# Optimization experiments

Hardware: AMD Instinct MI355X
Metric: run time of the kernel (lower is better)

Reference implementation:

```python
import jax, jax.numpy as jnp
import numpy as np

B, N, D, K, H, HID, ITERS = 16, 4096, 64, 8, 4, 256, 3
DH = D // H
EPS = 1e-5


def _ln(x, g, b):
    m = x.mean(-1, keepdims=True)
    v = x.var(-1, keepdims=True)
    return (x - m) / jnp.sqrt(v + EPS) * g + b


def setup_inputs() -> dict:
    ks = jax.random.split(jax.random.key(0), 16)
    s = 1.0 / np.sqrt(D)
    return {
        "embeddings": jax.random.normal(ks[0], (B, N, D), dtype=jnp.float32),
        "slots_mu": jax.random.normal(ks[1], (1, K, D), dtype=jnp.float32) * 0.1,
        "slots_logsigma": jax.random.normal(ks[2], (1, K, D), dtype=jnp.float32) * 0.1,
        "mixing_init": jnp.full((1, K), 1.0 / K, dtype=jnp.float32),
        "to_keys": jax.random.uniform(ks[3], (K, D, D), dtype=jnp.float32),
        "to_queries": jax.random.uniform(ks[4], (K, D, D), dtype=jnp.float32),
        "to_values": jax.random.uniform(ks[5], (K, D, D), dtype=jnp.float32),
        "w_ih": jax.random.uniform(ks[6], (3 * D, D), minval=-s, maxval=s),
        "w_hh": jax.random.uniform(ks[7], (3 * D, D), minval=-s, maxval=s),
        "b_ih": jax.random.uniform(ks[8], (3 * D,), minval=-s, maxval=s),
        "b_hh": jax.random.uniform(ks[9], (3 * D,), minval=-s, maxval=s),
        "w1": jax.random.uniform(ks[10], (HID, D), minval=-s, maxval=s),
        "b1": jnp.zeros((HID,), jnp.float32),
        "w2": jax.random.uniform(ks[11], (D, HID), minval=-1.0 / np.sqrt(HID), maxval=1.0 / np.sqrt(HID)),
        "b2": jnp.zeros((D,), jnp.float32),
        "ln_in_g": jnp.ones((D,), jnp.float32), "ln_in_b": jnp.zeros((D,), jnp.float32),
        "ln_sl_g": jnp.ones((D,), jnp.float32), "ln_sl_b": jnp.zeros((D,), jnp.float32),
        "ln_ff_g": jnp.ones((D,), jnp.float32), "ln_ff_b": jnp.zeros((D,), jnp.float32),
        "noise_init": jax.random.normal(ks[12], (B, K, D), dtype=jnp.float32),
        "noise_final": jax.random.normal(ks[13], (B, K, D), dtype=jnp.float32),
    }


def reference(embeddings, slots_mu, slots_logsigma, mixing_init, to_keys, to_queries,
              to_values, w_ih, w_hh, b_ih, b_hh, w1, b1, w2, b2,
              ln_in_g, ln_in_b, ln_sl_g, ln_sl_b, ln_ff_g, ln_ff_b,
              noise_init, noise_final):
    mu = jnp.broadcast_to(slots_mu, (B, K, D))
    sigma = jnp.broadcast_to(jnp.exp(slots_logsigma), (B, K, D))
    slots = mu + sigma * noise_init                              # [B,K,D]
    mixing = jnp.broadcast_to(mixing_init, (B, K))[:, :, None]   # [B,K,1]

    x = _ln(embeddings, ln_in_g, ln_in_b)                        # [B,N,D]
    keys = jnp.einsum('bne,ked->bknd', x, to_keys).reshape(B, K, N, H, DH)
    values = jnp.einsum('bne,ked->bknd', x, to_values).reshape(B, K, N, H, DH)
    sigma = sigma.reshape(B, K, H, DH)
    # torch.einsum('bkd,kdd->bkd') uses the DIAGONAL of to_queries
    qdiag = jnp.einsum('kdd->kd', to_queries)                    # [K,D]
    log_pi = -0.5 * D * np.log(2.0 * np.pi)

    attn_vis = None
    for _ in range(ITERS):
        slots_prev = slots
        s_ln = _ln(slots, ln_sl_g, ln_sl_b)
        queries = (s_ln * qdiag[None]).reshape(B, K, H, DH)      # [B,K,H,Dh]
        exponent = -0.5 * (keys - queries[:, :, None]) ** 2 / (sigma[:, :, None] ** 2 + EPS)
        log_scale = -jnp.log(jnp.clip(sigma, EPS, None))[:, :, None]  # [B,K,1,H,Dh]
        gll = jnp.log(mixing + EPS)[..., None] + (log_pi + log_scale + exponent).sum(-1)  # [B,K,N,H]
        attn = jax.nn.softmax(gll, axis=1) + EPS
        attn_vis = attn
        Nk = attn.sum(axis=(2, 3))[:, :, None]                   # [B,K,1]
        upd = jnp.einsum('bknh,bknhd->bkhd', attn, values).reshape(B, K, D)
        upd = (1.0 / Nk + EPS) * upd
        nq = upd.reshape(B, K, H, DH)                            # source overwrites new_queries with slot_updates
        sig2 = jnp.einsum('bknh,bknhd->bkhd', attn, (keys - nq[:, :, None]) ** 2).reshape(B, K, D)
        sigma = (jnp.sqrt(sig2 / Nk) + EPS).reshape(B, K, H, DH)
        mixing = Nk / N
        # GRUCell (torch gate order: reset, update, new)
        xg = upd.reshape(-1, D) @ w_ih.T + b_ih
        hg = slots_prev.reshape(-1, D) @ w_hh.T + b_hh
        xr, xz, xn = jnp.split(xg, 3, axis=-1)
        hr, hz, hn = jnp.split(hg, 3, axis=-1)
        r = jax.nn.sigmoid(xr + hr)
        z = jax.nn.sigmoid(xz + hz)
        n = jnp.tanh(xn + r * hn)
        slots = ((1.0 - z) * n + z * slots_prev.reshape(-1, D)).reshape(B, K, D)
        pre = _ln(slots, ln_ff_g, ln_ff_b)
        slots = slots + jax.nn.relu(pre @ w1.T + b1) @ w2.T + b2

    sigma = sigma.reshape(B, K, D)
    slots = slots + sigma * noise_final
    return slots, attn_vis
```

## Files before the change

### kernel.cpp

```cpp
#include <hip/hip_runtime.h>
#include <math.h>

#define B_ 16
#define N_ 4096
#define D_ 64
#define K_ 8
#define H_ 4
#define HID_ 256
#define ITERS_ 3
#define EPS_ 1e-5f

#define HTERM_ (-940.9930580015849f)

__device__ __forceinline__ float waveReduceSum64(float v) {
  v += __shfl_xor(v, 1);  v += __shfl_xor(v, 2);  v += __shfl_xor(v, 4);
  v += __shfl_xor(v, 8);  v += __shfl_xor(v, 16); v += __shfl_xor(v, 32);
  return v;
}
__device__ __forceinline__ float groupReduceSum16(float v) {
  v += __shfl_xor(v, 1); v += __shfl_xor(v, 2); v += __shfl_xor(v, 4);
  v += __shfl_xor(v, 8);
  return v;
}

template <int CTRL>
__device__ __forceinline__ float dpp_mov(float v) {
  return __int_as_float(__builtin_amdgcn_update_dpp(
      0, __float_as_int(v), CTRL, 0xF, 0xF, true));
}
__device__ __forceinline__ float row16Sum(float v) {
  v += dpp_mov<0xB1>(v);
  v += dpp_mov<0x4E>(v);
  v += dpp_mov<0x124>(v);
  v += dpp_mov<0x128>(v);
  return v;
}

__global__ __launch_bounds__(256) void key_kernel(const float* __restrict__ emb,
    const float* __restrict__ g_in, const float* __restrict__ b_in,
    const float* __restrict__ Wk, float* __restrict__ x,
    float* __restrict__ keys, int b0) {
  __shared__ float xst[64 * 68];
  __shared__ float wks[64 * 64];
  int n0 = blockIdx.x * 64;
  int bl = blockIdx.y;
  int tid = threadIdx.x;
  int wave = tid >> 6, lane = tid & 63;

  {
    const float* eb = emb + ((size_t)(b0 + bl) * N_ + n0 + wave * 16) * 64 + lane;
    float* xrow = x + ((size_t)bl * N_ + n0 + wave * 16) * 64 + lane;
    float gl = g_in[lane], bb = b_in[lane];
    #pragma unroll 4
    for (int r = 0; r < 16; ++r) {
      float e = eb[(size_t)r * 64];
      float s  = waveReduceSum64(e);
      float sq = waveReduceSum64(e * e);
      float mean = s * (1.0f / 64.0f);
      float var  = sq * (1.0f / 64.0f) - mean * mean;
      float xv = (e - mean) * rsqrtf(var + EPS_) * gl + bb;
      xst[lane * 68 + wave * 16 + r] = xv;
      xrow[(size_t)r * 64] = xv;
    }
  }

  int tr = tid >> 4, tc = tid & 15;
  int r0 = tr * 4, c0 = tc * 4;
  size_t outb = ((size_t)bl * N_ + n0) * 512;

  for (int k = 0; k < K_; ++k) {
    __syncthreads();
    const float4* wk4 = (const float4*)(Wk + (size_t)k * 4096);
    float4* wks4 = (float4*)wks;
    for (int i = tid; i < 1024; i += 256) wks4[i] = wk4[i];
    __syncthreads();

    float ak[4][4] = {{0.f}};
    #pragma unroll 8
    for (int kk = 0; kk < 64; ++kk) {
      float4 xq = *(const float4*)&xst[kk * 68 + r0];
      float4 wq = *(const float4*)&wks[kk * 64 + c0];
      float xv[4] = {xq.x, xq.y, xq.z, xq.w};
      float wc[4] = {wq.x, wq.y, wq.z, wq.w};
      #pragma unroll
      for (int i = 0; i < 4; ++i)
        #pragma unroll
        for (int j = 0; j < 4; ++j)
          ak[i][j] = fmaf(xv[i], wc[j], ak[i][j]);
    }
    size_t ob = outb + (size_t)k * 64;
    #pragma unroll
    for (int i = 0; i < 4; ++i) {
      float4 kq = make_float4(ak[i][0], ak[i][1], ak[i][2], ak[i][3]);
      *(float4*)&keys[ob + (size_t)(r0 + i) * 512 + c0] = kq;
    }
  }
}

__global__ void init_kernel(const float* __restrict__ mu, const float* __restrict__ lsig,
                            const float* __restrict__ mix0, const float* __restrict__ noise,
                            const float* __restrict__ tq,
                            const float* __restrict__ g_sl, const float* __restrict__ b_sl,
                            float* __restrict__ slots, float* __restrict__ q,
                            float* __restrict__ i2s, float* __restrict__ base,
                            float* __restrict__ S1, float* __restrict__ S2,
                            float* __restrict__ S0, float* __restrict__ T, int b0) {
  int bk = b0 * K_ + blockIdx.x;
  int lane = threadIdx.x;
  int k = bk & (K_ - 1);
  int kd = k * 64 + lane;
  float sg = expf(lsig[kd]);
  float s = mu[kd] + sg * noise[bk * 64 + lane];
  slots[bk * 64 + lane] = s;
  float su = waveReduceSum64(s);
  float sq = waveReduceSum64(s * s);
  float mean = su * (1.0f / 64.0f);
  float var  = sq * (1.0f / 64.0f) - mean * mean;
  float sl = (s - mean) * rsqrtf(var + EPS_) * g_sl[lane] + b_sl[lane];
  q[bk * 64 + lane] = sl * tq[k * 4096 + lane * 65];
  i2s[bk * 64 + lane] = 0.5f / (sg * sg + EPS_);
  float ls = -logf(fmaxf(sg, EPS_));
  float lss = groupReduceSum16(ls);
  if ((lane & 15) == 0)
    base[bk * 4 + (lane >> 4)] = logf(mix0[k] + EPS_) + HTERM_ + lss;
  S1[bk * 64 + lane] = 0.0f;
  S2[bk * 64 + lane] = 0.0f;
  T[bk * 256 + lane]       = 0.0f;
  T[bk * 256 + 64 + lane]  = 0.0f;
  T[bk * 256 + 128 + lane] = 0.0f;
  T[bk * 256 + 192 + lane] = 0.0f;
  if (lane < 4) S0[bk * 4 + lane] = 0.0f;
}

template <bool WRITE_ATTN>
__global__ __launch_bounds__(256, 4) void attn_kernel(
    const float* __restrict__ keys, const float* __restrict__ x,
    const float* __restrict__ q, const float* __restrict__ i2s, const float* __restrict__ base,
    float* __restrict__ S1, float* __restrict__ S2, float* __restrict__ S0,
    float* __restrict__ T, float* __restrict__ attn_out, int b0) {
  int bl = blockIdx.y;
  int bg = b0 + bl;
  int wave = threadIdx.x >> 6, lane = threadIdx.x & 63;
  int h = lane >> 4;
  int n0 = (blockIdx.x * 4 + wave) * 16;

  __shared__ float att_lds[4][K_][64];
  __shared__ float blk[3104];
  __shared__ float bv_lds[32];
  for (int i = threadIdx.x; i < 3104; i += 256) blk[i] = 0.0f;
  if (threadIdx.x < 32) bv_lds[threadIdx.x] = base[bg * 32 + threadIdx.x];

  float qv[K_], iv[K_];
  {
    const float* qp = q + bg * 512 + lane;
    const float* ip = i2s + bg * 512 + lane;
    #pragma unroll
    for (int k = 0; k < K_; ++k) { qv[k] = qp[k * 64]; iv[k] = ip[k * 64]; }
  }
  float s1a[K_] = {0.f}, s2a[K_] = {0.f};
  __syncthreads();

  const float* kptr = keys + ((size_t)bl * N_ + n0) * 512 + lane;
  #pragma unroll 2
  for (int ni = 0; ni < 16; ++ni) {
    float key[K_], gl[K_];
    #pragma unroll
    for (int k = 0; k < K_; ++k) key[k] = kptr[k * 64];
    #pragma unroll
    for (int k = 0; k < K_; ++k) {
      float df = key[k] - qv[k];
      float t = row16Sum(df * df * iv[k]);
      gl[k] = bv_lds[k * 4 + h] - t;
    }
    float m = gl[0];
    #pragma unroll
    for (int k = 1; k < K_; ++k) m = fmaxf(m, gl[k]);
    float ssum = 0.f;
    #pragma unroll
    for (int k = 0; k < K_; ++k) { gl[k] = __expf(gl[k] - m); ssum += gl[k]; }
    float inv = __builtin_amdgcn_rcpf(ssum);
    #pragma unroll
    for (int k = 0; k < K_; ++k) {
      float a = gl[k] * inv + EPS_;
      s1a[k] = fmaf(a, key[k], s1a[k]);
      s2a[k] = fmaf(a * key[k], key[k], s2a[k]);
      if ((lane & 15) == 0) att_lds[wave][k][ni * 4 + h] = a;
    }
    kptr += 512;
  }
  #pragma unroll
  for (int k = 0; k < K_; ++k) {
    atomicAdd(&blk[k * 64 + lane],       s1a[k]);
    atomicAdd(&blk[512 + k * 64 + lane], s2a[k]);
  }

  float xr[16];
  {
    const float* xptr = x + ((size_t)bl * N_ + n0) * 64 + lane;
    #pragma unroll
    for (int ni = 0; ni < 16; ++ni) xr[ni] = xptr[ni * 64];
  }
  #pragma unroll
  for (int k = 0; k < K_; ++k) {
    float t0 = 0.f, t1 = 0.f, t2 = 0.f, t3 = 0.f;
    float c0 = 0.f, c1 = 0.f, c2 = 0.f, c3 = 0.f;
    #pragma unroll
    for (int ni = 0; ni < 16; ++ni) {
      float4 a4 = *(const float4*)&att_lds[wave][k][ni * 4];
      float xv = xr[ni];
      t0 = fmaf(a4.x, xv, t0); t1 = fmaf(a4.y, xv, t1);
      t2 = fmaf(a4.z, xv, t2); t3 = fmaf(a4.w, xv, t3);
      c0 += a4.x; c1 += a4.y; c2 += a4.z; c3 += a4.w;
    }
    atomicAdd(&blk[1024 + k * 256 + lane],       t0);
    atomicAdd(&blk[1024 + k * 256 + 64 + lane],  t1);
    atomicAdd(&blk[1024 + k * 256 + 128 + lane], t2);
    atomicAdd(&blk[1024 + k * 256 + 192 + lane], t3);
    if (lane == 0) {
      atomicAdd(&blk[3072 + k * 4 + 0], c0);
      atomicAdd(&blk[3072 + k * 4 + 1], c1);
      atomicAdd(&blk[3072 + k * 4 + 2], c2);
      atomicAdd(&blk[3072 + k * 4 + 3], c3);
    }
  }
  __syncthreads();
  for (int i = threadIdx.x; i < 512; i += 256) {
    atomicAdd(&S1[bg * 512 + i], blk[i]);
    atomicAdd(&S2[bg * 512 + i], blk[512 + i]);
  }
  for (int i = threadIdx.x; i < 2048; i += 256)
    atomicAdd(&T[bg * 2048 + i], blk[1024 + i]);
  if (threadIdx.x < 32) atomicAdd(&S0[bg * 32 + threadIdx.x], blk[3072 + threadIdx.x]);
  if (WRITE_ATTN) {
    #pragma unroll
    for (int k = 0; k < K_; ++k)
      attn_out[((size_t)(bg * K_ + k) * N_ + n0) * 4 + lane] = att_lds[wave][k][lane];
  }
}

__global__ __launch_bounds__(64) void update_kernel(
    float* __restrict__ S1, float* __restrict__ S2,
    float* __restrict__ S0, float* __restrict__ T,
    const float* __restrict__ Wv,
    float* __restrict__ slots,
    const float* __restrict__ w_ih, const float* __restrict__ w_hh,
    const float* __restrict__ b_ih, const float* __restrict__ b_hh,
    const float* __restrict__ w1, const float* __restrict__ b1,
    const float* __restrict__ w2, const float* __restrict__ b2,
    const float* __restrict__ g_ff, const float* __restrict__ b_ff,
    const float* __restrict__ tq,
    const float* __restrict__ g_sl, const float* __restrict__ b_sl,
    float* __restrict__ q, float* __restrict__ i2s, float* __restrict__ base,
    const float* __restrict__ noise_final, float* __restrict__ out_slots,
    int last, int b0) {
  int bk = b0 * K_ + blockIdx.x;
  int k = bk & (K_ - 1);
  int t = threadIdx.x;
  __shared__ float upd_s[64], sp_s[64], pre_s[64], hid_s[256];

  float nk = S0[bk * 4 + 0] + S0[bk * 4 + 1] + S0[bk * 4 + 2] + S0[bk * 4 + 3];
  float sv = 0.f;
  {
    const float* Trow = T + bk * 256 + (t >> 4) * 64;
    const float* wv = Wv + (size_t)k * 4096 + t;
    #pragma unroll 8
    for (int e = 0; e < 64; ++e) sv = fmaf(Trow[e], wv[(size_t)e * 64], sv);
  }
  float upd = (1.0f / nk + EPS_) * sv;
  upd_s[t] = upd;
  float s1 = S1[bk * 64 + t], s2 = S2[bk * 64 + t], s0 = S0[bk * 4 + (t >> 4)];
  float sig2 = fmaxf(s2 - 2.0f * upd * s1 + upd * upd * s0, 0.0f);
  float sig = sqrtf(sig2 / nk) + EPS_;
  float sp = slots[bk * 64 + t];
  sp_s[t] = sp;
  S1[bk * 64 + t] = 0.0f;
  S2[bk * 64 + t] = 0.0f;
  T[bk * 256 + t]       = 0.0f;
  T[bk * 256 + 64 + t]  = 0.0f;
  T[bk * 256 + 128 + t] = 0.0f;
  T[bk * 256 + 192 + t] = 0.0f;
  if (t < 4) S0[bk * 4 + t] = 0.0f;

  float xr_ = b_ih[t], xz_ = b_ih[64 + t], xn_ = b_ih[128 + t];
  float hr_ = b_hh[t], hz_ = b_hh[64 + t], hn_ = b_hh[128 + t];
  {
    const float4* wr = (const float4*)(w_ih + t * 64);
    const float4* wz = (const float4*)(w_ih + (64 + t) * 64);
    const float4* wn = (const float4*)(w_ih + (128 + t) * 64);
    const float4* vr = (const float4*)(w_hh + t * 64);
    const float4* vz = (const float4*)(w_hh + (64 + t) * 64);
    const float4* vn = (const float4*)(w_hh + (128 + t) * 64);
    #pragma unroll
    for (int d4 = 0; d4 < 16; ++d4) {
      float4 u4 = *(const float4*)&upd_s[d4 * 4];
      float4 p4 = *(const float4*)&sp_s[d4 * 4];
      float4 a = wr[d4], b = wz[d4], c = wn[d4];
      float4 d = vr[d4], e = vz[d4], f = vn[d4];
      xr_ += u4.x * a.x + u4.y * a.y + u4.z * a.z + u4.w * a.w;
      xz_ += u4.x * b.x + u4.y * b.y + u4.z * b.z + u4.w * b.w;
      xn_ += u4.x * c.x + u4.y * c.y + u4.z * c.z + u4.w * c.w;
      hr_ += p4.x * d.x + p4.y * d.y + p4.z * d.z + p4.w * d.w;
      hz_ += p4.x * e.x + p4.y * e.y + p4.z * e.z + p4.w * e.w;
      hn_ += p4.x * f.x + p4.y * f.y + p4.z * f.z + p4.w * f.w;
    }
  }
  float r = 1.0f / (1.0f + expf(-(xr_ + hr_)));
  float z = 1.0f / (1.0f + expf(-(xz_ + hz_)));
  float nn = tanhf(xn_ + r * hn_);
  float sn = (1.0f - z) * nn + z * sp;

  {
    float su = waveReduceSum64(sn);
    float sq = waveReduceSum64(sn * sn);
    float mean = su * (1.0f / 64.0f);
    float var  = sq * (1.0f / 64.0f) - mean * mean;
    pre_s[t] = (sn - mean) * rsqrtf(var + EPS_) * g_ff[t] + b_ff[t];
  }

  {
    float a0 = b1[t * 4], a1 = b1[t * 4 + 1], a2 = b1[t * 4 + 2], a3 = b1[t * 4 + 3];
    const float4* w10 = (const float4*)(w1 + (t * 4) * 64);
    const float4* w11 = (const float4*)(w1 + (t * 4 + 1) * 64);
    const float4* w12 = (const float4*)(w1 + (t * 4 + 2) * 64);
    const float4* w13 = (const float4*)(w1 + (t * 4 + 3) * 64);
    #pragma unroll
    for (int d4 = 0; d4 < 16; ++d4) {
      float4 p4 = *(const float4*)&pre_s[d4 * 4];
      float4 a = w10[d4], b = w11[d4], c = w12[d4], d = w13[d4];
      a0 += p4.x * a.x + p4.y * a.y + p4.z * a.z + p4.w * a.w;
      a1 += p4.x * b.x + p4.y * b.y + p4.z * b.z + p4.w * b.w;
      a2 += p4.x * c.x + p4.y * c.y + p4.z * c.z + p4.w * c.w;
      a3 += p4.x * d.x + p4.y * d.y + p4.z * d.z + p4.w * d.w;
    }
    *(float4*)&hid_s[t * 4] = make_float4(fmaxf(a0, 0.f), fmaxf(a1, 0.f),
                                          fmaxf(a2, 0.f), fmaxf(a3, 0.f));
  }

  {
    float a = b2[t];
    const float4* w2r = (const float4*)(w2 + t * 256);
    #pragma unroll
    for (int j4 = 0; j4 < 64; ++j4) {
      float4 w = w2r[j4];
      float4 hh = *(const float4*)&hid_s[j4 * 4];
      a += hh.x * w.x + hh.y * w.y + hh.z * w.z + hh.w * w.w;
    }
    float outv = sn + a;
    slots[bk * 64 + t] = outv;
    if (last) {
      out_slots[bk * 64 + t] = outv + sig * noise_final[bk * 64 + t];
    } else {
      float su = waveReduceSum64(outv);
      float sq = waveReduceSum64(outv * outv);
      float mean = su * (1.0f / 64.0f);
      float var  = sq * (1.0f / 64.0f) - mean * mean;
      float sl = (outv - mean) * rsqrtf(var + EPS_) * g_sl[t] + b_sl[t];
      q[bk * 64 + t] = sl * tq[k * 4096 + t * 65];
      i2s[bk * 64 + t] = 0.5f / (sig * sig + EPS_);
      float ls = -logf(fmaxf(sig, EPS_));
      float lss = groupReduceSum16(ls);
      if ((t & 15) == 0)
        base[bk * 4 + (t >> 4)] = logf(nk * (1.0f / (float)N_) + EPS_) + HTERM_ + lss;
    }
  }
}

extern "C" void kernel_launch(void* const* d_in, const int* in_sizes, int n_in,
                              void* d_out, int out_size, void* d_ws, size_t ws_size,
                              hipStream_t stream) {
  const float* emb  = (const float*)d_in[0];
  const float* mu   = (const float*)d_in[1];
  const float* lsig = (const float*)d_in[2];
  const float* mix0 = (const float*)d_in[3];
  const float* Wk   = (const float*)d_in[4];
  const float* Wq   = (const float*)d_in[5];
  const float* Wv   = (const float*)d_in[6];
  const float* w_ih = (const float*)d_in[7];
  const float* w_hh = (const float*)d_in[8];
  const float* b_ih = (const float*)d_in[9];
  const float* b_hh = (const float*)d_in[10];
  const float* w1   = (const float*)d_in[11];
  const float* b1   = (const float*)d_in[12];
  const float* w2   = (const float*)d_in[13];
  const float* b2   = (const float*)d_in[14];
  const float* g_in = (const float*)d_in[15];
  const float* b_in = (const float*)d_in[16];
  const float* g_sl = (const float*)d_in[17];
  const float* b_sl = (const float*)d_in[18];
  const float* g_ff = (const float*)d_in[19];
  const float* b_ff = (const float*)d_in[20];
  const float* nz0  = (const float*)d_in[21];
  const float* nzf  = (const float*)d_in[22];

  float* ws = (float*)d_ws;
  float* slots = ws;
  float* q     = slots + 8192;
  float* i2s   = q + 8192;
  float* base  = i2s + 8192;
  float* S1    = base + 512;
  float* S2    = S1 + 8192;
  float* S0    = S2 + 8192;
  float* T     = S0 + 512;
  float* x     = T + 32768;
  const size_t small_bytes = (size_t)(5 * 8192 + 2 * 512 + 32768) * 4;
  const size_t per_batch = (size_t)(N_ * 64 + N_ * 512) * 4;

  int C = 16;
  while (C > 1 && small_bytes + (size_t)C * per_batch > ws_size) C >>= 1;
  float* keys = x + (size_t)C * N_ * 64;

  float* out_slots = (float*)d_out;
  float* out_attn  = out_slots + B_ * K_ * 64;

  for (int b0 = 0; b0 < B_; b0 += C) {
    key_kernel<<<dim3(N_ / 64, C), 256, 0, stream>>>(emb, g_in, b_in, Wk, x, keys, b0);
    init_kernel<<<dim3(C * K_), 64, 0, stream>>>(mu, lsig, mix0, nz0, Wq, g_sl, b_sl,
                                                 slots, q, i2s, base, S1, S2, S0, T, b0);
    for (int it = 0; it < ITERS_; ++it) {
      int last = (it == ITERS_ - 1) ? 1 : 0;
      if (last)
        attn_kernel<true><<<dim3(N_ / 64, C), 256, 0, stream>>>(keys, x, q, i2s, base,
                                                                S1, S2, S0, T, out_attn, b0);
      else
        attn_kernel<false><<<dim3(N_ / 64, C), 256, 0, stream>>>(keys, x, q, i2s, base,
                                                                 S1, S2, S0, T, nullptr, b0);
      update_kernel<<<dim3(C * K_), 64, 0, stream>>>(S1, S2, S0, T, Wv, slots,
          w_ih, w_hh, b_ih, b_hh, w1, b1, w2, b2, g_ff, b_ff,
          Wq, g_sl, b_sl, q, i2s, base, nzf, out_slots, last, b0);
    }
  }
}
```

Baseline: 472.3 us.

## Double-buffer key rows through LDS with async global-to-LDS loads in attn kernel

Replaces the direct per-lane global loads of key rows in the attention loop with a per-wave double-buffered LDS stage. Rows are filled with global_load_lds DMA two iterations ahead and synchronised with explicit vmcnt/lgkmcnt waits and scheduling barriers. The aim is to overlap key fetch latency with the softmax and accumulation work. In exchange it adds 16KB of LDS per block, which may reduce occupancy at 4 blocks per CU, and the hand-placed waitcnt/sched barriers may serialise the loop.

```diff
diff --git a/kernel.cpp b/kernel.cpp
--- a/kernel.cpp
+++ b/kernel.cpp
@@ -34,6 +34,21 @@
   v += dpp_mov<0x124>(v);
   v += dpp_mov<0x128>(v);
   return v;
+}
+
+__device__ __forceinline__ void stage_row(const float* rowg, float* ldsrow, int lane) {
+#if __has_builtin(__builtin_amdgcn_global_load_lds)
+  typedef __attribute__((address_space(1))) const float GF;
+  typedef __attribute__((address_space(3))) float LF;
+  __builtin_amdgcn_global_load_lds((GF*)(rowg + lane * 4),       (LF*)ldsrow,         16, 0, 0);
+  __builtin_amdgcn_global_load_lds((GF*)(rowg + 256 + lane * 4), (LF*)(ldsrow + 256), 16, 0, 0);
+#else
+  #pragma unroll
+  for (int j = 0; j < 4; ++j) {
+    ldsrow[lane * 4 + j]       = rowg[lane * 4 + j];
+    ldsrow[256 + lane * 4 + j] = rowg[256 + lane * 4 + j];
+  }
+#endif
 }
 
 __global__ __launch_bounds__(256) void key_kernel(const float* __restrict__ emb,
@@ -147,6 +162,7 @@
   __shared__ float att_lds[4][K_][64];
   __shared__ float blk[3104];
   __shared__ float bv_lds[32];
+  __shared__ __align__(16) float kbuf[4][2][512];
   for (int i = threadIdx.x; i < 3104; i += 256) blk[i] = 0.0f;
   if (threadIdx.x < 32) bv_lds[threadIdx.x] = base[bg * 32 + threadIdx.x];
 
@@ -160,12 +176,23 @@
   float s1a[K_] = {0.f}, s2a[K_] = {0.f};
   __syncthreads();
 
-  const float* kptr = keys + ((size_t)bl * N_ + n0) * 512 + lane;
-  #pragma unroll 2
+  const float* rowbase = keys + ((size_t)bl * N_ + n0) * 512;
+  stage_row(rowbase,       &kbuf[wave][0][0], lane);
+  stage_row(rowbase + 512, &kbuf[wave][1][0], lane);
   for (int ni = 0; ni < 16; ++ni) {
-    float key[K_], gl[K_];
-    #pragma unroll
-    for (int k = 0; k < K_; ++k) key[k] = kptr[k * 64];
+    if (ni < 15) { asm volatile("s_waitcnt vmcnt(2)" ::: "memory"); }
+    else         { asm volatile("s_waitcnt vmcnt(0)" ::: "memory"); }
+    __builtin_amdgcn_sched_barrier(0);
+    float key[K_];
+    const float* kb = &kbuf[wave][ni & 1][0];
+    #pragma unroll
+    for (int k = 0; k < K_; ++k) key[k] = kb[k * 64 + lane];
+    if (ni < 14) {
+      asm volatile("s_waitcnt lgkmcnt(0)" ::: "memory");
+      __builtin_amdgcn_sched_barrier(0);
+      stage_row(rowbase + (size_t)(ni + 2) * 512, &kbuf[wave][ni & 1][0], lane);
+    }
+    float gl[K_];
     #pragma unroll
     for (int k = 0; k < K_; ++k) {
       float df = key[k] - qv[k];
@@ -186,7 +213,6 @@
       s2a[k] = fmaf(a * key[k], key[k], s2a[k]);
       if ((lane & 15) == 0) att_lds[wave][k][ni * 4 + h] = a;
     }
-    kptr += 512;
   }
   #pragma unroll
   for (int k = 0; k < K_; ++k) {
```

Measured after the change: 478.8 us. About the same (+1.4%).
